# Performance work log

Measured on AMD Instinct MI355X. Metric: run time of the kernel, lower is better.

Reference implementation:

```python
import jax, jax.numpy as jnp
import numpy as np

N, E = 65536, 524288
IN_DIM, HID_DIM, OUT_DIM = 1024, 512, 256


def setup_inputs() -> dict:
    key = jax.random.key(0)
    k1, k2, k3, k4, k5, k6 = jax.random.split(key, 6)
    h = jax.random.normal(k1, (N, IN_DIM), dtype=jnp.float32)
    src = jax.random.randint(k2, (E,), 0, N, dtype=jnp.int64)
    dst = jax.random.randint(k3, (E,), 0, N, dtype=jnp.int64)
    # Glorot-uniform weights as in DGL GraphConv
    lim1 = float(np.sqrt(6.0 / (IN_DIM + HID_DIM)))
    lim2 = float(np.sqrt(6.0 / (HID_DIM + OUT_DIM)))
    W1 = jax.random.uniform(k4, (IN_DIM, HID_DIM), jnp.float32, -lim1, lim1)
    W2 = jax.random.uniform(k5, (HID_DIM, OUT_DIM), jnp.float32, -lim2, lim2)
    b1 = jnp.zeros((HID_DIM,), jnp.float32)
    b2 = jnp.zeros((OUT_DIM,), jnp.float32)
    return {"h": h, "W1": W1, "b1": b1, "W2": W2, "b2": b2, "src": src, "dst": dst}


def _graph_conv(x, W, b, src, dst, inv_sqrt_dout, inv_sqrt_din):
    # DGL GraphConv, norm='both': D_in^{-1/2} A D_out^{-1/2} X W + b
    # Apply dense transform first (in_dim >= out_dim path in DGL) -- same math.
    x = x * inv_sqrt_dout[:, None]
    x = x @ W  # [N, out]
    agg = jax.ops.segment_sum(x[src], dst, num_segments=x.shape[0])  # scatter-add over edges
    return agg * inv_sqrt_din[:, None] + b


def reference(h, W1, b1, W2, b2, src, dst):
    n = h.shape[0]
    ones = jnp.ones((src.shape[0],), h.dtype)
    deg_out = jnp.maximum(jax.ops.segment_sum(ones, src, num_segments=n), 1.0)
    deg_in = jnp.maximum(jax.ops.segment_sum(ones, dst, num_segments=n), 1.0)
    inv_sqrt_dout = jax.lax.rsqrt(deg_out)
    inv_sqrt_din = jax.lax.rsqrt(deg_in)
    x = _graph_conv(h, W1, b1, src, dst, inv_sqrt_dout, inv_sqrt_din)
    x = jax.nn.elu(x)  # act; dropout p=0 -> identity
    out = _graph_conv(x, W2, b2, src, dst, inv_sqrt_dout, inv_sqrt_din)
    return out  # last_act = Identity
```

## Files before the change

kernel.cpp:

```cpp
#include <hip/hip_runtime.h>
#include <hip/hip_bf16.h>

#define IN_DIM 1024
#define HID 512
#define OUTD 256

typedef __attribute__((ext_vector_type(8))) short short8;
typedef __attribute__((ext_vector_type(4))) float f32x4;
typedef __attribute__((ext_vector_type(8))) unsigned short ushort8e;
typedef __attribute__((ext_vector_type(4))) unsigned short ushort4e;

template<int F> struct VecSel;
template<> struct VecSel<8> { using T = ushort8e; };
template<> struct VecSel<4> { using T = ushort4e; };


__device__ inline unsigned short f2bf(float f) {
    union { float f; unsigned u; } v; v.f = f;
    unsigned r = (v.u + 0x7FFF + ((v.u >> 16) & 1)) >> 16;
    return (unsigned short)r;
}

__device__ inline float bf2f(unsigned short u) {
    union { unsigned u; float f; } v; v.u = ((unsigned)u) << 16; return v.f;
}

__device__ inline void gload16(const void* g, void* l) {
    __builtin_amdgcn_global_load_lds(
        (const __attribute__((address_space(1))) void*)g,
        (__attribute__((address_space(3))) void*)l, 16, 0, 0);
}


__global__ void deg_kernel(const int* __restrict__ src, const int* __restrict__ dst,
                           int* __restrict__ dego, int* __restrict__ degi, int E) {
    int i = blockIdx.x * blockDim.x + threadIdx.x;
    if (i < E) {
        atomicAdd(&dego[src[i]], 1);
        atomicAdd(&degi[dst[i]], 1);
    }
}

__global__ void invsqrt_kernel(const int* __restrict__ dego, const int* __restrict__ degi,
                               float* __restrict__ iso, float* __restrict__ isi, int n) {
    int i = blockIdx.x * blockDim.x + threadIdx.x;
    if (i < n) {
        iso[i] = rsqrtf(fmaxf((float)dego[i], 1.0f));
        isi[i] = rsqrtf(fmaxf((float)degi[i], 1.0f));
    }
}


__global__ __launch_bounds__(256) void scan_block(const int* __restrict__ deg,
                                                  int* __restrict__ excl,
                                                  int* __restrict__ partials) {
    __shared__ int tmp[256];
    int tid = threadIdx.x;
    int i = blockIdx.x * 256 + tid;
    int v = deg[i];
    tmp[tid] = v;
    __syncthreads();
    #pragma unroll
    for (int off = 1; off < 256; off <<= 1) {
        int t = (tid >= off) ? tmp[tid - off] : 0;
        __syncthreads();
        tmp[tid] += t;
        __syncthreads();
    }
    excl[i] = tmp[tid] - v;
    if (tid == 255) partials[blockIdx.x] = tmp[255];
}

__global__ __launch_bounds__(256) void scan_partials(int* __restrict__ partials) {
    __shared__ int tmp[256];
    int tid = threadIdx.x;
    int v = partials[tid];
    tmp[tid] = v;
    __syncthreads();
    #pragma unroll
    for (int off = 1; off < 256; off <<= 1) {
        int t = (tid >= off) ? tmp[tid - off] : 0;
        __syncthreads();
        tmp[tid] += t;
        __syncthreads();
    }
    partials[tid] = tmp[tid] - v;
}

__global__ __launch_bounds__(256) void scan_add(const int* __restrict__ excl,
                                                const int* __restrict__ partials,
                                                const int* __restrict__ deg,
                                                int* __restrict__ row_start,
                                                int* __restrict__ cursor, int n) {
    int i = blockIdx.x * 256 + threadIdx.x;
    int v = excl[i] + partials[blockIdx.x];
    row_start[i] = v;
    cursor[i] = v;
    if (i == n - 1) row_start[n] = v + deg[i];
}

__global__ void csr_fill(const int* __restrict__ src, const int* __restrict__ dst,
                         int* __restrict__ cursor, int* __restrict__ eidx, int E) {
    int e = blockIdx.x * blockDim.x + threadIdx.x;
    if (e < E) {
        int pos = atomicAdd(&cursor[dst[e]], 1);
        eidx[pos] = src[e];
    }
}


__global__ void transpose_cvt(const float* __restrict__ W, unsigned short* __restrict__ Wt,
                              int K, int N) {
    int i = blockIdx.x * 256 + threadIdx.x;
    if (i < N * K) {
        int n = i / K, k = i - n * K;
        Wt[i] = f2bf(W[(size_t)k * N + n]);
    }
}


__global__ __launch_bounds__(256) void gemm1_wide(
    const float* __restrict__ A, const unsigned short* __restrict__ Bt,
    const float* __restrict__ rowscale, unsigned short* __restrict__ Cb, int M)
{
    __shared__ unsigned short As[64][32];
    __shared__ unsigned short Bs[512][32];

    const int tid  = threadIdx.x;
    const int lane = tid & 63;
    const int wave = tid >> 6;
    const int lrow = lane & 15;
    const int lkg  = lane >> 4;

    const int m0 = blockIdx.x * 64;

    char* AsB = (char*)&As[0][0];
    char* BsB = (char*)&Bs[0][0];

    const int rA = tid >> 2;
    const int g  = tid & 3;
    const int qpA = g ^ ((rA >> 1) & 3);
    const float sc = rowscale[m0 + rA];

    const int rslot = (lkg ^ ((lrow >> 1) & 3)) * 8;

    f32x4 acc[4][8] = {};

    const int nk = IN_DIM / 32;
    for (int kt = 0; kt < nk; ++kt) {
        const int k0 = kt * 32;

        #pragma unroll
        for (int i = 0; i < 8; ++i) {
            const int s = i * 256 + wave * 64 + lane;
            const int r = s >> 2;
            const int q = (s & 3) ^ ((s >> 3) & 3);
            gload16(Bt + (size_t)r * IN_DIM + k0 + q * 8,
                    BsB + (i * 256 + wave * 64) * 16);
        }

        {
            const float* pa = A + (size_t)(m0 + rA) * IN_DIM + k0 + g * 8;
            float4 x = *reinterpret_cast<const float4*>(pa);
            float4 y = *reinterpret_cast<const float4*>(pa + 4);
            short8 kv;
            kv[0] = (short)f2bf(x.x * sc); kv[1] = (short)f2bf(x.y * sc);
            kv[2] = (short)f2bf(x.z * sc); kv[3] = (short)f2bf(x.w * sc);
            kv[4] = (short)f2bf(y.x * sc); kv[5] = (short)f2bf(y.y * sc);
            kv[6] = (short)f2bf(y.z * sc); kv[7] = (short)f2bf(y.w * sc);
            *reinterpret_cast<short8*>(AsB + rA * 64 + qpA * 16) = kv;
        }

        __syncthreads();

        short8 af[4], bfr[8];
        #pragma unroll
        for (int mi = 0; mi < 4; ++mi)
            af[mi] = *reinterpret_cast<const short8*>(&As[mi * 16 + lrow][rslot]);
        #pragma unroll
        for (int ni = 0; ni < 8; ++ni)
            bfr[ni] = *reinterpret_cast<const short8*>(&Bs[wave * 128 + ni * 16 + lrow][rslot]);

        #pragma unroll
        for (int mi = 0; mi < 4; ++mi)
            #pragma unroll
            for (int ni = 0; ni < 8; ++ni)
                acc[mi][ni] = __builtin_amdgcn_mfma_f32_16x16x32_bf16(
                    af[mi], bfr[ni], acc[mi][ni], 0, 0, 0);

        __syncthreads();
    }

    #pragma unroll
    for (int mi = 0; mi < 4; ++mi)
        #pragma unroll
        for (int ni = 0; ni < 8; ++ni)
            #pragma unroll
            for (int r = 0; r < 4; ++r)
                Cb[(size_t)(m0 + mi * 16 + lkg * 4 + r) * HID
                   + (wave * 128 + ni * 16 + lrow)] = f2bf(acc[mi][ni][r]);
}


#define TM 128
#define TN 128
#define TK 64
#define NXCD 8

__global__ __launch_bounds__(256) void gemm2_bf16(
    const unsigned short* __restrict__ Ab, const unsigned short* __restrict__ Bt,
    unsigned short* __restrict__ Cb, int M, int K, int Nc)
{
    __shared__ unsigned short As[2][TM][TK];
    __shared__ unsigned short Bs[2][TN][TK];

    const int tid  = threadIdx.x;
    const int lane = tid & 63;
    const int wave = tid >> 6;
    const int wr = wave >> 1, wc = wave & 1;
    const int lrow = lane & 15;
    const int lkg  = lane >> 4;

    const int nwg = gridDim.x;
    const int per = nwg / NXCD;
    const int lin = blockIdx.x;
    const int newlin = (lin % NXCD) * per + lin / NXCD;
    const int ncb = Nc / TN;
    const int m0 = (newlin / ncb) * TM;
    const int n0 = (newlin % ncb) * TN;

    int srow[4], sq[4];
    #pragma unroll
    for (int i = 0; i < 4; ++i) {
        int s = i * 256 + wave * 64 + lane;
        srow[i] = s >> 3;
        sq[i] = (s & 7) ^ ((s >> 3) & 7);
    }

    char* AsB = (char*)&As[0][0][0];
    char* BsB = (char*)&Bs[0][0][0];

    auto stageOp = [&](const unsigned short* G, int rc0, int kt, char* opBase, int buf) {
        const int k0 = kt * TK;
        #pragma unroll
        for (int i = 0; i < 4; ++i)
            gload16(G + (size_t)(rc0 + srow[i]) * K + k0 + sq[i] * 8,
                    opBase + buf * 16384 + (i * 256 + wave * 64) * 16);
    };

    f32x4 acc[4][4] = {};

    stageOp(Bt, n0, 0, BsB, 0);
    stageOp(Ab, m0, 0, AsB, 0);
    __syncthreads();

    const int nk = K / TK;
    for (int kt = 0; kt < nk; ++kt) {
        const int cur = kt & 1, nxt = cur ^ 1;

        if (kt + 1 < nk) {
            stageOp(Bt, n0, kt + 1, BsB, nxt);
            stageOp(Ab, m0, kt + 1, AsB, nxt);
        }

        #pragma unroll
        for (int ks = 0; ks < 2; ++ks) {
            short8 af[4], bfr[4];
            #pragma unroll
            for (int mi = 0; mi < 4; ++mi) {
                const int row = wr * 64 + mi * 16 + lrow;
                const int qp = (ks * 4 + lkg) ^ (lrow & 7);
                af[mi] = *reinterpret_cast<const short8*>(&As[cur][row][qp * 8]);
            }
            #pragma unroll
            for (int ni = 0; ni < 4; ++ni) {
                const int row = wc * 64 + ni * 16 + lrow;
                const int qp = (ks * 4 + lkg) ^ (lrow & 7);
                bfr[ni] = *reinterpret_cast<const short8*>(&Bs[cur][row][qp * 8]);
            }
            #pragma unroll
            for (int mi = 0; mi < 4; ++mi)
                #pragma unroll
                for (int ni = 0; ni < 4; ++ni)
                    acc[mi][ni] = __builtin_amdgcn_mfma_f32_16x16x32_bf16(
                        af[mi], bfr[ni], acc[mi][ni], 0, 0, 0);
        }

        __syncthreads();
    }

    #pragma unroll
    for (int mi = 0; mi < 4; ++mi)
        #pragma unroll
        for (int ni = 0; ni < 4; ++ni)
            #pragma unroll
            for (int r = 0; r < 4; ++r)
                Cb[(size_t)(m0 + wr * 64 + mi * 16 + lkg * 4 + r) * Nc
                   + (n0 + wc * 64 + ni * 16 + lrow)] = f2bf(acc[mi][ni][r]);
}


template<int DIM, bool LAYER1>
__global__ __launch_bounds__(256) void aggregate(
    const int* __restrict__ row_start, const int* __restrict__ eidx,
    const unsigned short* __restrict__ Xb, const float* __restrict__ isi,
    const float* __restrict__ iso, const float* __restrict__ bias,
    unsigned short* __restrict__ out_bf, float* __restrict__ out_f)
{
    constexpr int F = DIM / 64;
    using VecT = typename VecSel<F>::T;
    const int node = blockIdx.x * 4 + (threadIdx.x >> 6);
    const int lane = threadIdx.x & 63;

    const int beg = row_start[node];
    const int end = row_start[node + 1];
    const unsigned short* base = Xb + lane * F;

    float acc[F] = {};
    int e = beg;
    for (; e + 3 < end; e += 4) {
        int i0 = eidx[e], i1 = eidx[e + 1], i2 = eidx[e + 2], i3 = eidx[e + 3];
        VecT v0 = *reinterpret_cast<const VecT*>(base + (size_t)i0 * DIM);
        VecT v1 = *reinterpret_cast<const VecT*>(base + (size_t)i1 * DIM);
        VecT v2 = *reinterpret_cast<const VecT*>(base + (size_t)i2 * DIM);
        VecT v3 = *reinterpret_cast<const VecT*>(base + (size_t)i3 * DIM);
        #pragma unroll
        for (int f = 0; f < F; ++f) {
            acc[f] += bf2f(v0[f]); acc[f] += bf2f(v1[f]);
            acc[f] += bf2f(v2[f]); acc[f] += bf2f(v3[f]);
        }
    }
    for (; e < end; ++e) {
        VecT v0 = *reinterpret_cast<const VecT*>(base + (size_t)eidx[e] * DIM);
        #pragma unroll
        for (int f = 0; f < F; ++f) acc[f] += bf2f(v0[f]);
    }

    const float si = isi[node];
    float bv[F];
    #pragma unroll
    for (int q = 0; q < F / 4; ++q)
        *reinterpret_cast<float4*>(&bv[q * 4]) =
            *reinterpret_cast<const float4*>(bias + lane * F + q * 4);

    if (LAYER1) {
        const float so = iso[node];
        short8 o;
        #pragma unroll
        for (int f = 0; f < F; ++f) {
            float v = acc[f] * si + bv[f];
            v = v > 0.f ? v : expm1f(v);
            o[f] = (short)f2bf(v * so);
        }
        *reinterpret_cast<short8*>(out_bf + (size_t)node * DIM + lane * F) = o;
    } else {
        #pragma unroll
        for (int q = 0; q < F / 4; ++q) {
            float4 v = make_float4(acc[q * 4 + 0] * si + bv[q * 4 + 0],
                                   acc[q * 4 + 1] * si + bv[q * 4 + 1],
                                   acc[q * 4 + 2] * si + bv[q * 4 + 2],
                                   acc[q * 4 + 3] * si + bv[q * 4 + 3]);
            *reinterpret_cast<float4*>(out_f + (size_t)node * DIM + lane * F + q * 4) = v;
        }
    }
}


extern "C" void kernel_launch(void* const* d_in, const int* in_sizes, int n_in,
                              void* d_out, int out_size, void* d_ws, size_t ws_size,
                              hipStream_t stream) {
    const float* h  = (const float*)d_in[0];
    const float* W1 = (const float*)d_in[1];
    const float* b1 = (const float*)d_in[2];
    const float* W2 = (const float*)d_in[3];
    const float* b2 = (const float*)d_in[4];
    const int*   src = (const int*)d_in[5];
    const int*   dst = (const int*)d_in[6];

    const int N = in_sizes[0] / IN_DIM;
    const int E = in_sizes[5];
    float* out = (float*)d_out;

    int* dego      = (int*)d_ws;
    int* degi      = dego + N;
    int* excl      = degi + N;
    int* partials  = excl + N;
    int* row_start = partials + 256;
    int* cursor    = row_start + N + 64;
    int* eidx      = cursor + N;
    float* iso     = (float*)(eidx + E);
    float* isi     = iso + N;
    unsigned short* W1t = (unsigned short*)(isi + N);
    unsigned short* W2t = W1t + (size_t)IN_DIM * HID;
    unsigned short* X1b = W2t + (size_t)HID * OUTD;
    unsigned short* X2b = X1b;
    unsigned short* R2h = X1b + (size_t)N * HID;

    hipMemsetAsync(dego, 0, sizeof(int) * (size_t)2 * N, stream);

    deg_kernel<<<(E + 255) / 256, 256, 0, stream>>>(src, dst, dego, degi, E);
    invsqrt_kernel<<<(N + 255) / 256, 256, 0, stream>>>(dego, degi, iso, isi, N);

    scan_block<<<N / 256, 256, 0, stream>>>(degi, excl, partials);
    scan_partials<<<1, 256, 0, stream>>>(partials);
    scan_add<<<N / 256, 256, 0, stream>>>(excl, partials, degi, row_start, cursor, N);
    csr_fill<<<(E + 255) / 256, 256, 0, stream>>>(src, dst, cursor, eidx, E);

    transpose_cvt<<<(IN_DIM * HID + 255) / 256, 256, 0, stream>>>(W1, W1t, IN_DIM, HID);
    transpose_cvt<<<(HID * OUTD + 255) / 256, 256, 0, stream>>>(W2, W2t, HID, OUTD);

    gemm1_wide<<<N / 64, 256, 0, stream>>>(h, W1t, iso, X1b, N);
    aggregate<HID, true><<<N / 4, 256, 0, stream>>>(
        row_start, eidx, X1b, isi, iso, b1, R2h, nullptr);

    gemm2_bf16<<<(N / TM) * (OUTD / TN), 256, 0, stream>>>(
        R2h, W2t, X2b, N, HID, OUTD);
    aggregate<OUTD, false><<<N / 4, 256, 0, stream>>>(
        row_start, eidx, X2b, isi, iso, b2, nullptr, out);
}
```

Baseline: 462.9 us.

## Load fp32 A tiles directly to LDS and move row scale into aggregation

```diff
diff --git a/kernel.cpp b/kernel.cpp
--- a/kernel.cpp
+++ b/kernel.cpp
@@ -9,6 +9,7 @@
 typedef __attribute__((ext_vector_type(4))) float f32x4;
 typedef __attribute__((ext_vector_type(8))) unsigned short ushort8e;
 typedef __attribute__((ext_vector_type(4))) unsigned short ushort4e;
+typedef __attribute__((ext_vector_type(4))) unsigned int uint4e;
 
 template<int F> struct VecSel;
 template<> struct VecSel<8> { using T = ushort8e; };
@@ -23,6 +24,16 @@
 
 __device__ inline float bf2f(unsigned short u) {
     union { unsigned u; float f; } v; v.u = ((unsigned)u) << 16; return v.f;
+}
+
+__device__ inline unsigned pk2(float a, float b) {
+    unsigned ua = __float_as_uint(a) + 0x8000u;
+    unsigned ub = __float_as_uint(b) + 0x8000u;
+#if __has_builtin(__builtin_amdgcn_perm)
+    return __builtin_amdgcn_perm(ub, ua, 0x07060302u);
+#else
+    return (ua >> 16) | (ub & 0xFFFF0000u);
+#endif
 }
 
 __device__ inline void gload16(const void* g, void* l) {
@@ -119,72 +130,87 @@
 }
 
 
-__global__ __launch_bounds__(256) void gemm1_wide(
+#define NXCD 8
+
+__global__ __launch_bounds__(256) void gemm1_f32lds(
     const float* __restrict__ A, const unsigned short* __restrict__ Bt,
-    const float* __restrict__ rowscale, unsigned short* __restrict__ Cb, int M)
+    unsigned short* __restrict__ Cb, int M)
 {
-    __shared__ unsigned short As[64][32];
-    __shared__ unsigned short Bs[512][32];
+    constexpr int K  = IN_DIM;
+    constexpr int NC = HID;
+    __shared__ float          As[128][32];
+    __shared__ unsigned short Bs[128][32];
 
     const int tid  = threadIdx.x;
     const int lane = tid & 63;
     const int wave = tid >> 6;
+    const int wr = wave >> 1, wc = wave & 1;
     const int lrow = lane & 15;
     const int lkg  = lane >> 4;
 
-    const int m0 = blockIdx.x * 64;
+    const int per = gridDim.x / NXCD;
+    const int newlin = (blockIdx.x % NXCD) * per + blockIdx.x / NXCD;
+    const int ncb = NC / 128;
+    const int m0 = (newlin / ncb) * 128;
+    const int n0 = (newlin % ncb) * 128;
 
     char* AsB = (char*)&As[0][0];
     char* BsB = (char*)&Bs[0][0];
 
-    const int rA = tid >> 2;
-    const int g  = tid & 3;
-    const int qpA = g ^ ((rA >> 1) & 3);
-    const float sc = rowscale[m0 + rA];
-
-    const int rslot = (lkg ^ ((lrow >> 1) & 3)) * 8;
-
-    f32x4 acc[4][8] = {};
-
-    const int nk = IN_DIM / 32;
-    for (int kt = 0; kt < nk; ++kt) {
+    int arow[4], aq[4];
+    #pragma unroll
+    for (int i = 0; i < 4; ++i) {
+        int s = i * 256 + wave * 64 + lane;
+        arow[i] = s >> 3;
+        aq[i] = (s & 7) ^ ((s >> 3) & 7);
+    }
+    int brow[2], bq[2];
+    #pragma unroll
+    for (int i = 0; i < 2; ++i) {
+        int s = i * 256 + wave * 64 + lane;
+        brow[i] = s >> 2;
+        bq[i] = (s & 3) ^ ((s >> 3) & 3);
+    }
+
+    const int rslotB = (lkg ^ ((lrow >> 1) & 3)) * 8;
+
+    f32x4 acc[4][4] = {};
+
+    for (int kt = 0; kt < K / 32; ++kt) {
         const int k0 = kt * 32;
 
         #pragma unroll
-        for (int i = 0; i < 8; ++i) {
-            const int s = i * 256 + wave * 64 + lane;
-            const int r = s >> 2;
-            const int q = (s & 3) ^ ((s >> 3) & 3);
-            gload16(Bt + (size_t)r * IN_DIM + k0 + q * 8,
+        for (int i = 0; i < 4; ++i)
+            gload16(A + (size_t)(m0 + arow[i]) * K + k0 + aq[i] * 4,
+                    AsB + (i * 256 + wave * 64) * 16);
+        #pragma unroll
+        for (int i = 0; i < 2; ++i)
+            gload16(Bt + (size_t)(n0 + brow[i]) * K + k0 + bq[i] * 8,
                     BsB + (i * 256 + wave * 64) * 16);
-        }
-
-        {
-            const float* pa = A + (size_t)(m0 + rA) * IN_DIM + k0 + g * 8;
-            float4 x = *reinterpret_cast<const float4*>(pa);
-            float4 y = *reinterpret_cast<const float4*>(pa + 4);
-            short8 kv;
-            kv[0] = (short)f2bf(x.x * sc); kv[1] = (short)f2bf(x.y * sc);
-            kv[2] = (short)f2bf(x.z * sc); kv[3] = (short)f2bf(x.w * sc);
-            kv[4] = (short)f2bf(y.x * sc); kv[5] = (short)f2bf(y.y * sc);
-            kv[6] = (short)f2bf(y.z * sc); kv[7] = (short)f2bf(y.w * sc);
-            *reinterpret_cast<short8*>(AsB + rA * 64 + qpA * 16) = kv;
-        }
-
-        __syncthreads();
-
-        short8 af[4], bfr[8];
+
+        __syncthreads();
+
+        short8 af[4], bfr[4];
+        #pragma unroll
+        for (int mi = 0; mi < 4; ++mi) {
+            const int row = wr * 64 + mi * 16 + lrow;
+            const int p0 = (2 * lkg) ^ (row & 7);
+            const int p1 = (2 * lkg + 1) ^ (row & 7);
+            f32x4 a0 = *reinterpret_cast<const f32x4*>(&As[row][p0 * 4]);
+            f32x4 a1 = *reinterpret_cast<const f32x4*>(&As[row][p1 * 4]);
+            uint4e u;
+            u[0] = pk2(a0[0], a0[1]); u[1] = pk2(a0[2], a0[3]);
+            u[2] = pk2(a1[0], a1[1]); u[3] = pk2(a1[2], a1[3]);
+            af[mi] = *reinterpret_cast<short8*>(&u);
+        }
+        #pragma unroll
+        for (int ni = 0; ni < 4; ++ni)
+            bfr[ni] = *reinterpret_cast<const short8*>(&Bs[wc * 64 + ni * 16 + lrow][rslotB]);
+
         #pragma unroll
         for (int mi = 0; mi < 4; ++mi)
-            af[mi] = *reinterpret_cast<const short8*>(&As[mi * 16 + lrow][rslot]);
-        #pragma unroll
-        for (int ni = 0; ni < 8; ++ni)
-            bfr[ni] = *reinterpret_cast<const short8*>(&Bs[wave * 128 + ni * 16 + lrow][rslot]);
-
-        #pragma unroll
-        for (int mi = 0; mi < 4; ++mi)
-            #pragma unroll
-            for (int ni = 0; ni < 8; ++ni)
+            #pragma unroll
+            for (int ni = 0; ni < 4; ++ni)
                 acc[mi][ni] = __builtin_amdgcn_mfma_f32_16x16x32_bf16(
                     af[mi], bfr[ni], acc[mi][ni], 0, 0, 0);
 
@@ -194,18 +220,17 @@
     #pragma unroll
     for (int mi = 0; mi < 4; ++mi)
         #pragma unroll
-        for (int ni = 0; ni < 8; ++ni)
+        for (int ni = 0; ni < 4; ++ni)
             #pragma unroll
             for (int r = 0; r < 4; ++r)
-                Cb[(size_t)(m0 + mi * 16 + lkg * 4 + r) * HID
-                   + (wave * 128 + ni * 16 + lrow)] = f2bf(acc[mi][ni][r]);
+                Cb[(size_t)(m0 + wr * 64 + mi * 16 + lkg * 4 + r) * NC
+                   + (n0 + wc * 64 + ni * 16 + lrow)] = f2bf(acc[mi][ni][r]);
 }
 
 
 #define TM 128
 #define TN 128
 #define TK 64
-#define NXCD 8
 
 __global__ __launch_bounds__(256) void gemm2_bf16(
     const unsigned short* __restrict__ Ab, const unsigned short* __restrict__ Bt,
@@ -221,10 +246,8 @@
     const int lrow = lane & 15;
     const int lkg  = lane >> 4;
 
-    const int nwg = gridDim.x;
-    const int per = nwg / NXCD;
-    const int lin = blockIdx.x;
-    const int newlin = (lin % NXCD) * per + lin / NXCD;
+    const int per = gridDim.x / NXCD;
+    const int newlin = (blockIdx.x % NXCD) * per + blockIdx.x / NXCD;
     const int ncb = Nc / TN;
     const int m0 = (newlin / ncb) * TM;
     const int n0 = (newlin % ncb) * TN;
@@ -320,20 +343,32 @@
     int e = beg;
     for (; e + 3 < end; e += 4) {
         int i0 = eidx[e], i1 = eidx[e + 1], i2 = eidx[e + 2], i3 = eidx[e + 3];
+        float s0 = 1.f, s1 = 1.f, s2 = 1.f, s3 = 1.f;
+        if (LAYER1) { s0 = iso[i0]; s1 = iso[i1]; s2 = iso[i2]; s3 = iso[i3]; }
         VecT v0 = *reinterpret_cast<const VecT*>(base + (size_t)i0 * DIM);
         VecT v1 = *reinterpret_cast<const VecT*>(base + (size_t)i1 * DIM);
         VecT v2 = *reinterpret_cast<const VecT*>(base + (size_t)i2 * DIM);
         VecT v3 = *reinterpret_cast<const VecT*>(base + (size_t)i3 * DIM);
         #pragma unroll
         for (int f = 0; f < F; ++f) {
-            acc[f] += bf2f(v0[f]); acc[f] += bf2f(v1[f]);
-            acc[f] += bf2f(v2[f]); acc[f] += bf2f(v3[f]);
+            if (LAYER1) {
+                acc[f] = fmaf(s0, bf2f(v0[f]), acc[f]);
+                acc[f] = fmaf(s1, bf2f(v1[f]), acc[f]);
+                acc[f] = fmaf(s2, bf2f(v2[f]), acc[f]);
+                acc[f] = fmaf(s3, bf2f(v3[f]), acc[f]);
+            } else {
+                acc[f] += bf2f(v0[f]); acc[f] += bf2f(v1[f]);
+                acc[f] += bf2f(v2[f]); acc[f] += bf2f(v3[f]);
+            }
         }
     }
     for (; e < end; ++e) {
-        VecT v0 = *reinterpret_cast<const VecT*>(base + (size_t)eidx[e] * DIM);
-        #pragma unroll
-        for (int f = 0; f < F; ++f) acc[f] += bf2f(v0[f]);
+        int i0 = eidx[e];
+        float s0 = LAYER1 ? iso[i0] : 1.f;
+        VecT v0 = *reinterpret_cast<const VecT*>(base + (size_t)i0 * DIM);
+        #pragma unroll
+        for (int f = 0; f < F; ++f)
+            acc[f] = LAYER1 ? fmaf(s0, bf2f(v0[f]), acc[f]) : acc[f] + bf2f(v0[f]);
     }
 
     const float si = isi[node];
@@ -409,7 +444,7 @@
     transpose_cvt<<<(IN_DIM * HID + 255) / 256, 256, 0, stream>>>(W1, W1t, IN_DIM, HID);
     transpose_cvt<<<(HID * OUTD + 255) / 256, 256, 0, stream>>>(W2, W2t, HID, OUTD);
 
-    gemm1_wide<<<N / 64, 256, 0, stream>>>(h, W1t, iso, X1b, N);
+    gemm1_f32lds<<<(N / 128) * (HID / 128), 256, 0, stream>>>(h, W1t, X1b, N);
     aggregate<HID, true><<<N / 4, 256, 0, stream>>>(
         row_start, eidx, X1b, isi, iso, b1, R2h, nullptr);
 
```

New measurement: 402.4 us. -13.1%, faster.
